# Kernel optimization log

Hardware: AMD Instinct MI355X
Metric: run time of the kernel (lower is better)

Reference implementation:

```python
import jax, jax.numpy as jnp
import numpy as np
from jax import lax

K, C, H, W = 5, 256, 64, 64
NH, HD, P = 8, 32, 16           # heads, head_dim, patch_number
H0, W0 = 512, 512               # original mask resolution
SCALE_BASE = HD ** (-0.5)
GN_EPS = 1e-5


def _l2norm(x):
    n = jnp.sqrt(jnp.sum(x * x, axis=-1, keepdims=True))
    return x / jnp.maximum(n, 1e-12)


def _conv(x, w, b, pad):
    y = lax.conv_general_dilated(x, w, (1, 1), [(pad, pad), (pad, pad)],
                                 dimension_numbers=('NCHW', 'OIHW', 'NCHW'))
    return y + b[None, :, None, None]


def _group_norm(x, scale, bias, groups=4):
    n, c, h, w = x.shape
    xg = x.reshape(n, groups, -1)
    mu = jnp.mean(xg, axis=-1, keepdims=True)
    var = jnp.var(xg, axis=-1, keepdims=True)
    xg = (xg - mu) / jnp.sqrt(var + GN_EPS)
    return xg.reshape(n, c, h, w) * scale[None, :, None, None] + bias[None, :, None, None]


def setup_inputs() -> dict:
    key = jax.random.key(0)
    ks = jax.random.split(key, 16)
    x = jax.random.normal(ks[0], (1 + K, C, H, W), dtype=jnp.float32)
    delta = (jax.random.uniform(ks[1], (K, 1, H0, W0)) < 0.3).astype(jnp.float32)
    w = lambda k, sh: jax.random.normal(k, sh, dtype=jnp.float32) * 0.02
    return {
        'x': x, 'delta_onehot_x': delta,
        'Wq': w(ks[2], (C, C)), 'bq': jnp.zeros((C,), jnp.float32),
        'Ws': w(ks[3], (C, C)), 'bs': jnp.zeros((C,), jnp.float32),
        'scale': jnp.array(1.0, jnp.float32),
        'c1w': w(ks[4], (16, NH, 5, 5)), 'c1b': jnp.zeros((16,), jnp.float32),
        'g1s': jnp.ones((16,), jnp.float32), 'g1b': jnp.zeros((16,), jnp.float32),
        'c2w': w(ks[5], (64, 16, 3, 3)), 'c2b': jnp.zeros((64,), jnp.float32),
        'g2s': jnp.ones((64,), jnp.float32), 'g2b': jnp.zeros((64,), jnp.float32),
        'c3w': w(ks[6], (128, 64, 3, 3)), 'c3b': jnp.zeros((128,), jnp.float32),
        'g3s': jnp.ones((128,), jnp.float32), 'g3b': jnp.zeros((128,), jnp.float32),
    }


def reference(x, delta_onehot_x, Wq, bq, Ws, bs, scale,
              c1w, c1b, g1s, g1b, c2w, c2b, g2s, g2b, c3w, c3b, g3s, g3b):
    q = jnp.transpose(x[:1], (0, 2, 3, 1))    # [1,H,W,C]
    s = jnp.transpose(x[1:], (0, 2, 3, 1))    # [K,H,W,C]

    # nearest interpolation (torch 'nearest': src = floor(dst*in/out))
    ih = (jnp.arange(H) * H0) // H
    iw = (jnp.arange(W) * W0) // W
    d = delta_onehot_x[:, :, ih][:, :, :, iw]  # [K,1,H,W]

    q = (q @ Wq.T + bq).reshape(H, W, NH, HD).transpose(2, 0, 1, 3)        # [h,H,W,d]
    s = (s @ Ws.T + bs).reshape(K, H, W, NH, HD).transpose(0, 3, 1, 2, 4)  # [K,h,H,W,d]
    q = _l2norm(q) * scale * SCALE_BASE
    s = _l2norm(s)

    Hp, Wp = H // P, W // P
    S = P * P
    fg = d.reshape(K, P, Hp, P, Wp).transpose(0, 1, 3, 2, 4).reshape(K, S, Hp * Wp)
    bg = 1.0 - fg
    fg_sum = jnp.sum(fg, axis=-1)  # [K,S]
    bg_sum = jnp.sum(bg, axis=-1)

    sp = s.reshape(K, NH, P, Hp, P, Wp, HD).transpose(0, 1, 2, 4, 3, 5, 6)
    sp = sp.reshape(K, NH, S, Hp * Wp, HD)

    cs_fg = _l2norm(jnp.einsum('ksl,khsld->khsd', fg, sp))
    cs_bg = _l2norm(jnp.einsum('ksl,khsld->khsd', bg, sp))
    c_s = jnp.concatenate([cs_fg, cs_bg], axis=2).transpose(1, 0, 2, 3).reshape(NH, K * 2 * S, HD)
    c_v = jnp.concatenate([jnp.ones((K, NH, S), q.dtype), jnp.zeros((K, NH, S), q.dtype)],
                          axis=2).transpose(1, 0, 2).reshape(NH, K * 2 * S)

    mask = jnp.concatenate([jnp.where(fg_sum < 1.0, -jnp.inf, 0.0),
                            jnp.where(bg_sum < 1.0, -jnp.inf, 0.0)], axis=1)  # [K,2S]
    mask = mask.reshape(1, 1, 1, -1)

    attn = jax.nn.softmax(jnp.einsum('hyxd,hsd->hyxs', q, c_s) + mask, axis=-1)
    xo = jnp.einsum('hyxs,hs->hyx', attn, c_v)[None]  # [1,h,H,W]

    out = jax.nn.relu(_group_norm(_conv(xo, c1w, c1b, 2), g1s, g1b))
    out = jax.nn.relu(_group_norm(_conv(out, c2w, c2b, 1), g2s, g2b))
    out = jax.nn.relu(_group_norm(_conv(out, c3w, c3b, 1), g3s, g3b))
    return out
```

## Files before the change

### kernel.cpp

```cpp
#include <hip/hip_runtime.h>
#include <hip/hip_bf16.h>
#include <cstddef>

#define HW 4096

typedef __attribute__((ext_vector_type(8))) short bf16x8;
typedef __attribute__((ext_vector_type(4))) float f32x4;

__device__ __forceinline__ unsigned short f2b(float v) {
  __hip_bfloat16 b = __float2bfloat16(v);
  return *reinterpret_cast<unsigned short*>(&b);
}
__device__ __forceinline__ float b2f(unsigned short u) {
  return __bfloat162float(*reinterpret_cast<const __hip_bfloat16*>(&u));
}

__global__ __launch_bounds__(256) void txp_kernel(const float* __restrict__ x,
                                                  unsigned short* __restrict__ xb) {
  const int n = blockIdx.z, p0 = blockIdx.x * 64, ci0 = blockIdx.y * 64;
  const int t = threadIdx.x;
  __shared__ float Tl[64][65];
#pragma unroll
  for (int pass = 0; pass < 16; ++pass) {
    int ci = pass * 4 + (t >> 6), px = t & 63;
    Tl[ci][px] = x[((size_t)n * 256 + ci0 + ci) * HW + p0 + px];
  }
  __syncthreads();
#pragma unroll
  for (int pass = 0; pass < 16; ++pass) {
    int px = pass * 4 + (t >> 6), ci = t & 63;
    xb[((size_t)n * HW + p0 + px) * 256 + ci0 + ci] = f2b(Tl[ci][px]);
  }
}

__global__ __launch_bounds__(256) void wcv_kernel(const float* __restrict__ Wq,
                                                  const float* __restrict__ Ws,
                                                  unsigned short* __restrict__ wb) {
  int i = blockIdx.x * 256 + threadIdx.x;
  const float* W = (i < 65536) ? Wq : Ws;
  wb[i] = f2b(W[i & 65535]);
}

__global__ __launch_bounds__(256) void proj_kernel(
    const unsigned short* __restrict__ xb, const unsigned short* __restrict__ wb,
    const float* __restrict__ bq, const float* __restrict__ bs,
    const float* __restrict__ scale,
    unsigned short* __restrict__ qb, unsigned short* __restrict__ sb) {
  const int row0 = blockIdx.x * 128;
  const int n    = row0 >> 12;
  const int co0  = blockIdx.y * 64;
  const int t    = threadIdx.x;
  const int wv   = t >> 6;
  const int l    = t & 63;
  const float* __restrict__ B = (n == 0) ? bq : bs;
  const unsigned short* __restrict__ Wb = wb + (size_t)(n == 0 ? 0 : 1) * 65536;
  const int prow = row0 + wv * 32;

  const size_t ar0 = ((size_t)prow + (l & 15)) * 256 + (l >> 4) * 8;
  const size_t ar1 = ar0 + 16 * 256;
  size_t br[4];
#pragma unroll
  for (int b = 0; b < 4; ++b)
    br[b] = ((size_t)(co0 + b * 16 + (l & 15))) * 256 + (l >> 4) * 8;

  f32x4 acc[2][4];
#pragma unroll
  for (int a = 0; a < 2; ++a)
#pragma unroll
    for (int b = 0; b < 4; ++b) acc[a][b] = (f32x4){0.f, 0.f, 0.f, 0.f};

#pragma unroll
  for (int kc = 0; kc < 8; ++kc) {
    bf16x8 a0 = *(const bf16x8*)&xb[ar0 + kc * 32];
    bf16x8 a1 = *(const bf16x8*)&xb[ar1 + kc * 32];
#pragma unroll
    for (int b = 0; b < 4; ++b) {
      bf16x8 bb = *(const bf16x8*)&Wb[br[b] + kc * 32];
      acc[0][b] = __builtin_amdgcn_mfma_f32_16x16x32_bf16(a0, bb, acc[0][b], 0, 0, 0);
      acc[1][b] = __builtin_amdgcn_mfma_f32_16x16x32_bf16(a1, bb, acc[1][b], 0, 0, 0);
    }
  }

  float bias[4];
#pragma unroll
  for (int b = 0; b < 4; ++b) bias[b] = B[co0 + b * 16 + (l & 15)];
  const float qsc = scale[0] * 0.17677669529663687f;

#pragma unroll
  for (int a = 0; a < 2; ++a) {
#pragma unroll
    for (int r = 0; r < 4; ++r) {
      float v0 = acc[a][0][r] + bias[0];
      float v1 = acc[a][1][r] + bias[1];
      float v2 = acc[a][2][r] + bias[2];
      float v3 = acc[a][3][r] + bias[3];
      float s0 = v0 * v0 + v1 * v1;
      float s1 = v2 * v2 + v3 * v3;
#pragma unroll
      for (int m = 1; m <= 8; m <<= 1) {
        s0 += __shfl_xor(s0, m);
        s1 += __shfl_xor(s1, m);
      }
      float n0 = fmaxf(sqrtf(s0), 1e-12f);
      float n1 = fmaxf(sqrtf(s1), 1e-12f);
      v0 /= n0; v1 /= n0; v2 /= n1; v3 /= n1;
      const int px = prow + a * 16 + (l >> 4) * 4 + r;
      if (n == 0) {
        size_t o = (size_t)px * 256 + co0 + (l & 15);
        qb[o +  0] = f2b(v0 * qsc);
        qb[o + 16] = f2b(v1 * qsc);
        qb[o + 32] = f2b(v2 * qsc);
        qb[o + 48] = f2b(v3 * qsc);
      } else {
        size_t so = ((size_t)(px - 4096)) * 256 + co0 + (l & 15);
        sb[so +  0] = f2b(v0);
        sb[so + 16] = f2b(v1);
        sb[so + 32] = f2b(v2);
        sb[so + 48] = f2b(v3);
      }
    }
  }
}

__global__ __launch_bounds__(256) void agg_kernel(
    const float* __restrict__ delta, const unsigned short* __restrict__ sb,
    unsigned short* __restrict__ cb, float* __restrict__ mask) {
  const int s = blockIdx.x;
  const int k = blockIdx.y;
  const int t = threadIdx.x;
  __shared__ float fgl[16];
  const int sy = (s >> 4) * 4, sx = (s & 15) * 4;
  if (t < 16) {
    int y0 = (sy + (t >> 2)) * 8, x0 = (sx + (t & 3)) * 8;
    fgl[t] = delta[(size_t)k * 512 * 512 + (size_t)y0 * 512 + x0];
  }
  __syncthreads();
  const int h = t >> 5, d = t & 31;
  float af = 0.f, ab = 0.f;
#pragma unroll
  for (int l = 0; l < 16; ++l) {
    int pix = (sy + (l >> 2)) * 64 + sx + (l & 3);
    float sv = b2f(sb[((size_t)k * HW + pix) * 256 + h * 32 + d]);
    float f = fgl[l];
    af += f * sv;
    ab += (1.f - f) * sv;
  }
  float ssf = af * af, ssb = ab * ab;
#pragma unroll
  for (int m = 1; m <= 16; m <<= 1) {
    ssf += __shfl_xor(ssf, m);
    ssb += __shfl_xor(ssb, m);
  }
  float vf = af / fmaxf(sqrtf(ssf), 1e-12f);
  float vb = ab / fmaxf(sqrtf(ssb), 1e-12f);
  const int jf = k * 512 + s, jb = jf + 256;
  cb[((size_t)h * 2560 + jf) * 32 + d] = f2b(vf);
  cb[((size_t)h * 2560 + jb) * 32 + d] = f2b(vb);
  if (t == 0) {
    float fs = 0.f;
#pragma unroll
    for (int l = 0; l < 16; ++l) fs += fgl[l];
    mask[jf] = (fs < 1.f) ? -1e30f : 0.f;
    mask[jb] = ((16.f - fs) < 1.f) ? -1e30f : 0.f;
  }
}

__global__ __launch_bounds__(256) void attn_kernel(
    const unsigned short* __restrict__ qb, const unsigned short* __restrict__ cb,
    const float* __restrict__ mask, float* __restrict__ xo) {
  const int t = threadIdx.x;
  const int wv = t >> 6;
  const int l = t & 63;
  const int h = blockIdx.y;
  const int p0 = blockIdx.x * 64 + wv * 16;

  __shared__ float ml[2560];
  for (int i = t; i < 2560; i += 256) ml[i] = mask[i];

  const bf16x8 a = *(const bf16x8*)&qb[(size_t)(p0 + (l & 15)) * 256 + h * 32 + (l >> 4) * 8];
  __syncthreads();

  float num[4] = {0.f, 0.f, 0.f, 0.f}, den[4] = {0.f, 0.f, 0.f, 0.f};
  const size_t cbase = (size_t)h * 2560 * 32 + ((size_t)(l >> 4)) * 8;

  for (int j0 = 0; j0 < 2560; j0 += 16) {
    bf16x8 b = *(const bf16x8*)&cb[cbase + (size_t)(j0 + (l & 15)) * 32];
    f32x4 dacc = {0.f, 0.f, 0.f, 0.f};
    dacc = __builtin_amdgcn_mfma_f32_16x16x32_bf16(a, b, dacc, 0, 0, 0);
    float m = ml[j0 + (l & 15)];
    float cv = ((j0 & 511) < 256) ? 1.f : 0.f;
#pragma unroll
    for (int r = 0; r < 4; ++r) {
      float e = __expf(dacc[r] + m);
      den[r] += e;
      num[r] += cv * e;
    }
  }

#pragma unroll
  for (int r = 0; r < 4; ++r) {
#pragma unroll
    for (int msk = 1; msk <= 8; msk <<= 1) {
      den[r] += __shfl_xor(den[r], msk);
      num[r] += __shfl_xor(num[r], msk);
    }
  }
  if ((l & 15) == 0) {
#pragma unroll
    for (int r = 0; r < 4; ++r) {
      int px = p0 + (l >> 4) * 4 + r;
      xo[(size_t)h * HW + px] = num[r] / den[r];
    }
  }
}

__global__ __launch_bounds__(256) void conv1_stats(
    const float* __restrict__ in, const float* __restrict__ w,
    const float* __restrict__ b, float* __restrict__ out, float* __restrict__ stp) {
  const int t = threadIdx.x;
  const int y0 = blockIdx.x * 2;
  const int co0 = blockIdx.y * 2;
  __shared__ float Xl[8][6][68];
  __shared__ float Wl[8][25][2];
  __shared__ float sh[256], sh2[256];

  for (int idx = t; idx < 8 * 6 * 68; idx += 256) {
    int ci = idx / 408, rem = idx % 408, pr = rem / 68, pc = rem % 68;
    int iy = y0 + pr - 2, ix = pc - 2;
    float v = 0.f;
    if (iy >= 0 && iy < 64 && ix >= 0 && ix < 64) v = in[(size_t)ci * HW + iy * 64 + ix];
    Xl[ci][pr][pc] = v;
  }
  for (int idx = t; idx < 400; idx += 256) {
    int ci = idx / 50, rem = idx % 50, kk = rem / 2, c = rem % 2;
    Wl[ci][kk][c] = w[(size_t)((co0 + c) * 8 + ci) * 25 + kk];
  }
  __syncthreads();

  const int co_s = t >> 7, yr = (t >> 6) & 1, xi = t & 63;
  float acc = b[co0 + co_s];
#pragma unroll
  for (int ci = 0; ci < 8; ++ci)
#pragma unroll
    for (int ky = 0; ky < 5; ++ky)
#pragma unroll
      for (int kx = 0; kx < 5; ++kx)
        acc += Xl[ci][yr + ky][xi + kx] * Wl[ci][ky * 5 + kx][co_s];
  out[(size_t)(co0 + co_s) * HW + (y0 + yr) * 64 + xi] = acc;

  sh[t] = acc; sh2[t] = acc * acc;
  __syncthreads();
  for (int w2 = 128; w2 > 0; w2 >>= 1) {
    if (t < w2) { sh[t] += sh[t + w2]; sh2[t] += sh2[t + w2]; }
    __syncthreads();
  }
  if (t == 0) {
    int bid = blockIdx.y * 32 + blockIdx.x;
    stp[bid * 2] = sh[0]; stp[bid * 2 + 1] = sh2[0];
  }
}

__global__ __launch_bounds__(256) void conv2_gn(
    const float* __restrict__ t1, const float* __restrict__ stp1,
    const float* __restrict__ g1s, const float* __restrict__ g1b,
    const float* __restrict__ w, const float* __restrict__ b,
    float* __restrict__ t2, float* __restrict__ stp2) {
  const int t = threadIdx.x;
  const int y0 = blockIdx.x * 4;
  const int co0 = blockIdx.y * 4;
  __shared__ float Xl[16][6][66];
  __shared__ float Wl[16][9][4];
  __shared__ float gstat[4][2];
  __shared__ float sh[256], sh2[256];

  {
    int g = t >> 6, i = t & 63;
    float s = stp1[(g * 64 + i) * 2], ss = stp1[(g * 64 + i) * 2 + 1];
#pragma unroll
    for (int m = 1; m <= 32; m <<= 1) { s += __shfl_xor(s, m); ss += __shfl_xor(ss, m); }
    if (i == 0) {
      float nn = 4.f * HW;
      float mean = s / nn, var = ss / nn - mean * mean;
      gstat[g][0] = mean;
      gstat[g][1] = 1.f / sqrtf(var + 1e-5f);
    }
  }
  __syncthreads();

  for (int idx = t; idx < 16 * 6 * 66; idx += 256) {
    int ci = idx / 396, rem = idx % 396, pr = rem / 66, pc = rem % 66;
    int iy = y0 + pr - 1, ix = pc - 1;
    float v = 0.f;
    if (iy >= 0 && iy < 64 && ix >= 0 && ix < 64) {
      float raw = t1[(size_t)ci * HW + iy * 64 + ix];
      v = fmaxf((raw - gstat[ci >> 2][0]) * gstat[ci >> 2][1] * g1s[ci] + g1b[ci], 0.f);
    }
    Xl[ci][pr][pc] = v;
  }
  for (int idx = t; idx < 16 * 9 * 4; idx += 256) {
    int ci = idx / 36, rem = idx % 36, kk = rem / 4, c = rem % 4;
    Wl[ci][kk][c] = w[(size_t)((co0 + c) * 16 + ci) * 9 + kk];
  }
  __syncthreads();

  const int xi = t & 63, yr = t >> 6;
  float acc[4] = {b[co0], b[co0 + 1], b[co0 + 2], b[co0 + 3]};
#pragma unroll
  for (int ci = 0; ci < 16; ++ci)
#pragma unroll
    for (int ky = 0; ky < 3; ++ky)
#pragma unroll
      for (int kx = 0; kx < 3; ++kx) {
        float xv = Xl[ci][yr + ky][xi + kx];
        float4 wv = *(const float4*)&Wl[ci][ky * 3 + kx][0];
        acc[0] += xv * wv.x; acc[1] += xv * wv.y;
        acc[2] += xv * wv.z; acc[3] += xv * wv.w;
      }
  const int p = (y0 + yr) * 64 + xi;
  float s = 0.f, ss = 0.f;
#pragma unroll
  for (int c = 0; c < 4; ++c) {
    t2[(size_t)(co0 + c) * HW + p] = acc[c];
    s += acc[c]; ss += acc[c] * acc[c];
  }
  sh[t] = s; sh2[t] = ss;
  __syncthreads();
  for (int w2 = 128; w2 > 0; w2 >>= 1) {
    if (t < w2) { sh[t] += sh[t + w2]; sh2[t] += sh2[t + w2]; }
    __syncthreads();
  }
  if (t == 0) {
    int bid = blockIdx.y * 16 + blockIdx.x;
    stp2[bid * 2] = sh[0]; stp2[bid * 2 + 1] = sh2[0];
  }
}

__global__ __launch_bounds__(256) void conv3_gn(
    const float* __restrict__ t2, const float* __restrict__ stp2,
    const float* __restrict__ g2s, const float* __restrict__ g2b,
    const float* __restrict__ w, float* __restrict__ pp) {
  const int t = threadIdx.x;
  const int y0 = blockIdx.x * 4;
  const int co0 = blockIdx.y * 8;
  const int z = blockIdx.z;
  const int cb0 = z * 16;
  __shared__ float Xl[16][6][66];
  __shared__ float Wl[16][9][8];
  __shared__ float gm, gr;

  if (t < 64) {
    float s = stp2[(z * 64 + t) * 2], ss = stp2[(z * 64 + t) * 2 + 1];
#pragma unroll
    for (int m = 1; m <= 32; m <<= 1) { s += __shfl_xor(s, m); ss += __shfl_xor(ss, m); }
    if (t == 0) {
      float nn = 16.f * HW;
      float mean = s / nn, var = ss / nn - mean * mean;
      gm = mean;
      gr = 1.f / sqrtf(var + 1e-5f);
    }
  }
  __syncthreads();

  for (int idx = t; idx < 16 * 6 * 66; idx += 256) {
    int ci = idx / 396, rem = idx % 396, pr = rem / 66, pc = rem % 66;
    int iy = y0 + pr - 1, ix = pc - 1;
    float v = 0.f;
    if (iy >= 0 && iy < 64 && ix >= 0 && ix < 64) {
      float raw = t2[(size_t)(cb0 + ci) * HW + iy * 64 + ix];
      v = fmaxf((raw - gm) * gr * g2s[cb0 + ci] + g2b[cb0 + ci], 0.f);
    }
    Xl[ci][pr][pc] = v;
  }
  for (int idx = t; idx < 16 * 9 * 8; idx += 256) {
    int ci = idx / 72, rem = idx % 72, kk = rem / 8, c = rem % 8;
    Wl[ci][kk][c] = w[(size_t)((co0 + c) * 64 + cb0 + ci) * 9 + kk];
  }
  __syncthreads();

  const int xi = t & 63, yr = t >> 6;
  float acc[8] = {0.f, 0.f, 0.f, 0.f, 0.f, 0.f, 0.f, 0.f};
#pragma unroll
  for (int ci = 0; ci < 16; ++ci)
#pragma unroll
    for (int ky = 0; ky < 3; ++ky)
#pragma unroll
      for (int kx = 0; kx < 3; ++kx) {
        float xv = Xl[ci][yr + ky][xi + kx];
        const float4* w4 = (const float4*)&Wl[ci][ky * 3 + kx][0];
        float4 w0 = w4[0], w1 = w4[1];
        acc[0] += xv * w0.x; acc[1] += xv * w0.y; acc[2] += xv * w0.z; acc[3] += xv * w0.w;
        acc[4] += xv * w1.x; acc[5] += xv * w1.y; acc[6] += xv * w1.z; acc[7] += xv * w1.w;
      }
  const int p = (y0 + yr) * 64 + xi;
  float* o = pp + (size_t)z * 128 * HW;
#pragma unroll
  for (int c = 0; c < 8; ++c)
    o[(size_t)(co0 + c) * HW + p] = acc[c];
}

__global__ __launch_bounds__(256) void merge_stats(
    const float* __restrict__ pp, const float* __restrict__ b,
    float* __restrict__ out, float* __restrict__ stp, int S, int CO) {
  __shared__ float sh[256], sh2[256];
  const int t = threadIdx.x;
  const int idx = blockIdx.x * 256 + t;
  const int c = idx >> 12;
  float v = b[c];
  const size_t stride = (size_t)CO * HW;
  for (int s = 0; s < S; ++s) v += pp[(size_t)s * stride + idx];
  out[idx] = v;
  sh[t] = v; sh2[t] = v * v;
  __syncthreads();
  for (int w = 128; w > 0; w >>= 1) {
    if (t < w) { sh[t] += sh[t + w]; sh2[t] += sh2[t + w]; }
    __syncthreads();
  }
  if (t == 0) { stp[blockIdx.x * 2] = sh[0]; stp[blockIdx.x * 2 + 1] = sh2[0]; }
}

__global__ __launch_bounds__(256) void gn_apply(
    const float* __restrict__ in, float* __restrict__ out, const float* __restrict__ stp,
    const float* __restrict__ gs, const float* __restrict__ gb, int cpg, int bpg) {
  __shared__ float sh[256], sh2[256];
  const int t = threadIdx.x;
  const int idx = blockIdx.x * 256 + t;
  const int c = idx >> 12;
  const int g = c / cpg;
  float s = 0.f, ss = 0.f;
  for (int i = t; i < bpg; i += 256) {
    s  += stp[(g * bpg + i) * 2];
    ss += stp[(g * bpg + i) * 2 + 1];
  }
  sh[t] = s; sh2[t] = ss;
  __syncthreads();
  for (int w = 128; w > 0; w >>= 1) {
    if (t < w) { sh[t] += sh[t + w]; sh2[t] += sh2[t + w]; }
    __syncthreads();
  }
  const float nn = (float)(cpg * HW);
  const float mean = sh[0] / nn;
  const float var = sh2[0] / nn - mean * mean;
  const float rstd = 1.0f / sqrtf(var + 1e-5f);
  float v = (in[idx] - mean) * rstd * gs[c] + gb[c];
  out[idx] = fmaxf(v, 0.f);
}

extern "C" void kernel_launch(void* const* d_in, const int* in_sizes, int n_in,
                              void* d_out, int out_size, void* d_ws, size_t ws_size,
                              hipStream_t stream) {
  const float* x     = (const float*)d_in[0];
  const float* delta = (const float*)d_in[1];
  const float* Wq    = (const float*)d_in[2];
  const float* bq    = (const float*)d_in[3];
  const float* Ws    = (const float*)d_in[4];
  const float* bs    = (const float*)d_in[5];
  const float* scale = (const float*)d_in[6];
  const float* c1w = (const float*)d_in[7],  *c1b = (const float*)d_in[8];
  const float* g1s = (const float*)d_in[9],  *g1b = (const float*)d_in[10];
  const float* c2w = (const float*)d_in[11], *c2b = (const float*)d_in[12];
  const float* g2s = (const float*)d_in[13], *g2b = (const float*)d_in[14];
  const float* c3w = (const float*)d_in[15], *c3b = (const float*)d_in[16];
  const float* g3s = (const float*)d_in[17], *g3b = (const float*)d_in[18];

  float* ws = (float*)d_ws;
  unsigned short* sb = (unsigned short*)ws;
  unsigned short* xb = (unsigned short*)(ws + 2621440);
  unsigned short* qb = (unsigned short*)(ws + 5767168);
  unsigned short* cb = (unsigned short*)(ws + 6291456);
  float* mask = ws + 6619136;
  float* xo   = mask + 2560;
  float* stp1 = xo + 32768;
  float* stp2 = stp1 + 512;
  float* stp3 = stp2 + 512;
  unsigned short* wb = (unsigned short*)(stp3 + 4096);
  float* pp = ws;
  float* t1 = ws + 2097152;
  float* t2 = t1 + 65536;
  float* t3 = t2 + 262144;

  txp_kernel<<<dim3(64, 4, 6), 256, 0, stream>>>(x, xb);
  wcv_kernel<<<512, 256, 0, stream>>>(Wq, Ws, wb);
  proj_kernel<<<dim3(192, 4), 256, 0, stream>>>(xb, wb, bq, bs, scale, qb, sb);
  agg_kernel<<<dim3(256, 5), 256, 0, stream>>>(delta, sb, cb, mask);
  attn_kernel<<<dim3(64, 8), 256, 0, stream>>>(qb, cb, mask, xo);

  conv1_stats<<<dim3(32, 8), 256, 0, stream>>>(xo, c1w, c1b, t1, stp1);
  conv2_gn<<<dim3(16, 16), 256, 0, stream>>>(t1, stp1, g1s, g1b, c2w, c2b, t2, stp2);
  conv3_gn<<<dim3(16, 16, 4), 256, 0, stream>>>(t2, stp2, g2s, g2b, c3w, pp);
  merge_stats<<<2048, 256, 0, stream>>>(pp, c3b, t3, stp3, 4, 128);
  gn_apply<<<2048, 256, 0, stream>>>(t3, (float*)d_out, stp3, g3s, g3b, 32, 512);
}
```

Measured before the change: 127.6 us.

## Fuse NCHW transpose and bf16 conversion into projection kernel via LDS staging

Removes the separate transpose kernel and its bf16 scratch buffer. The projection kernel now reads fp32 x directly, converts it to bf16 and stages it in shared memory in MFMA fragment order. Each block handles 32 pixels across all 256 output channels, with one wave per 64-channel slice. This saves a launch and a global write plus read of the transposed activations. In exchange the per-block loads are narrower and strided, and the Af shared-memory writes may hit bank conflicts.

After: 122.3 us. 1.04x faster.

```diff
diff --git a/kernel.cpp b/kernel.cpp
--- a/kernel.cpp
+++ b/kernel.cpp
@@ -13,24 +13,6 @@
 }
 __device__ __forceinline__ float b2f(unsigned short u) {
   return __bfloat162float(*reinterpret_cast<const __hip_bfloat16*>(&u));
-}
-
-__global__ __launch_bounds__(256) void txp_kernel(const float* __restrict__ x,
-                                                  unsigned short* __restrict__ xb) {
-  const int n = blockIdx.z, p0 = blockIdx.x * 64, ci0 = blockIdx.y * 64;
-  const int t = threadIdx.x;
-  __shared__ float Tl[64][65];
-#pragma unroll
-  for (int pass = 0; pass < 16; ++pass) {
-    int ci = pass * 4 + (t >> 6), px = t & 63;
-    Tl[ci][px] = x[((size_t)n * 256 + ci0 + ci) * HW + p0 + px];
-  }
-  __syncthreads();
-#pragma unroll
-  for (int pass = 0; pass < 16; ++pass) {
-    int px = pass * 4 + (t >> 6), ci = t & 63;
-    xb[((size_t)n * HW + p0 + px) * 256 + ci0 + ci] = f2b(Tl[ci][px]);
-  }
 }
 
 __global__ __launch_bounds__(256) void wcv_kernel(const float* __restrict__ Wq,
@@ -42,22 +24,31 @@
 }
 
 __global__ __launch_bounds__(256) void proj_kernel(
-    const unsigned short* __restrict__ xb, const unsigned short* __restrict__ wb,
+    const float* __restrict__ x, const unsigned short* __restrict__ wb,
     const float* __restrict__ bq, const float* __restrict__ bs,
     const float* __restrict__ scale,
     unsigned short* __restrict__ qb, unsigned short* __restrict__ sb) {
-  const int row0 = blockIdx.x * 128;
+  const int row0 = blockIdx.x * 32;
   const int n    = row0 >> 12;
-  const int co0  = blockIdx.y * 64;
+  const int pxg  = row0 & 4095;
   const int t    = threadIdx.x;
   const int wv   = t >> 6;
   const int l    = t & 63;
+  const int co0  = wv * 64;
   const float* __restrict__ B = (n == 0) ? bq : bs;
   const unsigned short* __restrict__ Wb = wb + (size_t)(n == 0 ? 0 : 1) * 65536;
-  const int prow = row0 + wv * 32;
-
-  const size_t ar0 = ((size_t)prow + (l & 15)) * 256 + (l >> 4) * 8;
-  const size_t ar1 = ar0 + 16 * 256;
+
+  __shared__ unsigned short Af[2][8][64][8];
+
+#pragma unroll
+  for (int pass = 0; pass < 32; ++pass) {
+    int idx = pass * 256 + t;
+    int px = idx & 31, ci = idx >> 5;
+    float v = x[((size_t)n * 256 + ci) * HW + pxg + px];
+    Af[px >> 4][ci >> 5][((ci >> 3) & 3) * 16 + (px & 15)][ci & 7] = f2b(v);
+  }
+  __syncthreads();
+
   size_t br[4];
 #pragma unroll
   for (int b = 0; b < 4; ++b)
@@ -71,8 +62,8 @@
 
 #pragma unroll
   for (int kc = 0; kc < 8; ++kc) {
-    bf16x8 a0 = *(const bf16x8*)&xb[ar0 + kc * 32];
-    bf16x8 a1 = *(const bf16x8*)&xb[ar1 + kc * 32];
+    bf16x8 a0 = *(const bf16x8*)&Af[0][kc][l][0];
+    bf16x8 a1 = *(const bf16x8*)&Af[1][kc][l][0];
 #pragma unroll
     for (int b = 0; b < 4; ++b) {
       bf16x8 bb = *(const bf16x8*)&Wb[br[b] + kc * 32];
@@ -104,15 +95,15 @@
       float n0 = fmaxf(sqrtf(s0), 1e-12f);
       float n1 = fmaxf(sqrtf(s1), 1e-12f);
       v0 /= n0; v1 /= n0; v2 /= n1; v3 /= n1;
-      const int px = prow + a * 16 + (l >> 4) * 4 + r;
+      const int pix = pxg + a * 16 + (l >> 4) * 4 + r;
       if (n == 0) {
-        size_t o = (size_t)px * 256 + co0 + (l & 15);
+        size_t o = (size_t)pix * 256 + co0 + (l & 15);
         qb[o +  0] = f2b(v0 * qsc);
         qb[o + 16] = f2b(v1 * qsc);
         qb[o + 32] = f2b(v2 * qsc);
         qb[o + 48] = f2b(v3 * qsc);
       } else {
-        size_t so = ((size_t)(px - 4096)) * 256 + co0 + (l & 15);
+        size_t so = ((size_t)(n - 1) * HW + pix) * 256 + co0 + (l & 15);
         sb[so +  0] = f2b(v0);
         sb[so + 16] = f2b(v1);
         sb[so + 32] = f2b(v2);
@@ -464,7 +455,6 @@
 
   float* ws = (float*)d_ws;
   unsigned short* sb = (unsigned short*)ws;
-  unsigned short* xb = (unsigned short*)(ws + 2621440);
   unsigned short* qb = (unsigned short*)(ws + 5767168);
   unsigned short* cb = (unsigned short*)(ws + 6291456);
   float* mask = ws + 6619136;
@@ -478,9 +468,8 @@
   float* t2 = t1 + 65536;
   float* t3 = t2 + 262144;
 
-  txp_kernel<<<dim3(64, 4, 6), 256, 0, stream>>>(x, xb);
   wcv_kernel<<<512, 256, 0, stream>>>(Wq, Ws, wb);
-  proj_kernel<<<dim3(192, 4), 256, 0, stream>>>(xb, wb, bq, bs, scale, qb, sb);
+  proj_kernel<<<768, 256, 0, stream>>>(x, wb, bq, bs, scale, qb, sb);
   agg_kernel<<<dim3(256, 5), 256, 0, stream>>>(delta, sb, cb, mask);
   attn_kernel<<<dim3(64, 8), 256, 0, stream>>>(qb, cb, mask, xo);
 
```
